# Kernel tuning notes

Hardware: AMD Instinct MI355X
Metric: run time of the kernel (lower is better)

Reference implementation:

```python
import jax, jax.numpy as jnp
import numpy as np

B_, C_, H_, W_, Dd_ = 2, 64, 32, 32, 32
D_INNER, D_STATE, DT_RANK, D_CONV = 64, 8, 4, 4


def setup_inputs() -> dict:
    key = jax.random.key(0)
    ks = jax.random.split(key, 12)
    s = 0.05
    A_init = jnp.log(jnp.tile(jnp.arange(1, D_STATE + 1, dtype=jnp.float32), (D_INNER, 1)))
    return {
        "input": jax.random.normal(ks[0], (B_, C_, H_, W_, Dd_), jnp.float32),
        "conv_w": jax.random.normal(ks[1], (C_, C_, 3, 3, 3), jnp.float32) * s,
        "conv_b": jax.random.normal(ks[2], (C_,), jnp.float32) * s,
        "in_proj_w": jax.random.normal(ks[3], (2 * D_INNER, C_), jnp.float32) * s,
        "conv1d_w": jax.random.normal(ks[4], (D_INNER, 1, D_CONV), jnp.float32) * s,
        "conv1d_b": jax.random.normal(ks[5], (D_INNER,), jnp.float32) * s,
        "x_proj_w": jax.random.normal(ks[6], (DT_RANK + 2 * D_STATE, D_INNER), jnp.float32) * s,
        "dt_proj_w": jax.random.normal(ks[7], (D_INNER, DT_RANK), jnp.float32) * s,
        "dt_proj_b": jax.random.normal(ks[8], (D_INNER,), jnp.float32) * s,
        "A_log": A_init,
        "A_b_log": A_init + 0.01,
        "D_skip": jnp.ones((D_INNER,), jnp.float32),
        "out_proj_w": jax.random.normal(ks[9], (C_, D_INNER), jnp.float32) * s,
        "ln_g": jnp.ones((C_,), jnp.float32),
        "ln_b": jnp.zeros((C_,), jnp.float32),
    }


def _conv3d(x, w, b):
    y = jax.lax.conv_general_dilated(x, w, (1, 1, 1), [(1, 1), (1, 1), (1, 1)],
                                     dimension_numbers=("NCDHW", "OIDHW", "NCDHW"))
    return y + b[None, :, None, None, None]


def _instance_norm(x, eps=1e-5):
    m = x.mean(axis=(2, 3, 4), keepdims=True)
    v = ((x - m) ** 2).mean(axis=(2, 3, 4), keepdims=True)
    return (x - m) * jax.lax.rsqrt(v + eps)


def _selective_scan(xc, dt, Bm, Cm, A, D_skip):
    # xc, dt: (b,L,d); Bm, Cm: (b,L,n); A: (d,n)
    dA = jnp.exp(dt[..., None] * A)                       # (b,L,d,n)
    dBx = (dt * xc)[..., None] * Bm[:, :, None, :]        # (b,L,d,n)

    def comb(l, r):
        al, bl = l
        ar, br = r
        return ar * al, ar * bl + br

    _, h = jax.lax.associative_scan(comb, (dA, dBx), axis=1)
    y = jnp.einsum("bldn,bln->bld", h, Cm)
    return y + xc * D_skip


def _direction(xz, conv1d_w, conv1d_b, x_proj_w, dt_proj_w, dt_proj_b, A, D_skip):
    x, z = jnp.split(xz, 2, axis=-1)                      # each (b,L,d)
    xt = jnp.swapaxes(x, 1, 2)                            # (b,d,L)
    xc = jax.lax.conv_general_dilated(xt, conv1d_w, (1,), [(D_CONV - 1, 0)],
                                      feature_group_count=D_INNER,
                                      dimension_numbers=("NCH", "OIH", "NCH"))
    xc = jax.nn.silu(jnp.swapaxes(xc + conv1d_b[None, :, None], 1, 2))  # (b,L,d)
    dbl = xc @ x_proj_w.T
    dt_r = dbl[..., :DT_RANK]
    Bm = dbl[..., DT_RANK:DT_RANK + D_STATE]
    Cm = dbl[..., DT_RANK + D_STATE:]
    dt = jax.nn.softplus(dt_r @ dt_proj_w.T + dt_proj_b)
    y = _selective_scan(xc, dt, Bm, Cm, A, D_skip)
    return y * jax.nn.silu(z)


def reference(input, conv_w, conv_b, in_proj_w, conv1d_w, conv1d_b, x_proj_w,
              dt_proj_w, dt_proj_b, A_log, A_b_log, D_skip, out_proj_w, ln_g, ln_b):
    # skip path: Conv3d -> InstanceNorm3d -> ReLU
    skip = jax.nn.relu(_instance_norm(_conv3d(input, conv_w, conv_b)))
    b, c, h, w, d = input.shape
    tokens = input.transpose(0, 2, 3, 4, 1).reshape(b, h * w * d, c)  # b (hwd) c
    xz = tokens @ in_proj_w.T                                          # (b,L,2d)
    A = -jnp.exp(A_log)
    A_b = -jnp.exp(A_b_log)
    y_f = _direction(xz, conv1d_w, conv1d_b, x_proj_w, dt_proj_w, dt_proj_b, A, D_skip)
    y_b = _direction(xz[:, ::-1], conv1d_w, conv1d_b, x_proj_w, dt_proj_w, dt_proj_b, A_b, D_skip)[:, ::-1]
    out = ((y_f + y_b) @ out_proj_w.T) / 2.0  # if_devide_out=True
    mu = out.mean(-1, keepdims=True)
    var = ((out - mu) ** 2).mean(-1, keepdims=True)
    out = (out - mu) * jax.lax.rsqrt(var + 1e-5) * ln_g + ln_b  # use_norm=True
    vol = out.reshape(b, h, w, d, c).transpose(0, 4, 1, 2, 3)
    return _conv3d(vol, conv_w, conv_b) + skip
```

## Files before the change

### kernel.cpp

```cpp
#include <hip/hip_runtime.h>
#include <hip/hip_bf16.h>

typedef __hip_bfloat16 bf16;
typedef __attribute__((ext_vector_type(8))) short short8;
typedef __attribute__((ext_vector_type(4))) float f32x4;

__device__ __forceinline__ float b2f(bf16 x){ return __bfloat162float(x); }
__device__ __forceinline__ bf16  f2b(float x){ return __float2bfloat16(x); }
__device__ __forceinline__ float s2f(short s){ bf16 t = *(bf16*)&s; return b2f(t); }

__device__ __forceinline__ float ldin(const void* p, size_t i, int f32){
  return f32 ? ((const float*)p)[i] : b2f(((const bf16*)p)[i]);
}
__device__ __forceinline__ void stout(void* p, size_t i, float v, int f32){
  if(f32) ((float*)p)[i] = v; else ((bf16*)p)[i] = f2b(v);
}

constexpr int SP   = 32*32*32;
constexpr int LTOK = SP;
constexpr int NC   = 512;
constexpr int CLEN = LTOK / NC;
constexpr int NSEQ = 2*2*64*8;
constexpr int SEG  = 16;
constexpr int SEGLEN = NC/SEG;

__global__ void k_detect(const void* conv_w, int* flag){
  if(threadIdx.x==0 && blockIdx.x==0){
    const bf16* p = (const bf16*)conv_w;
    int f = 0;
    for(int i=0;i<128;i++){
      float v = b2f(p[i]);
      if(!(v==v) || fabsf(v) > 1.0f) f = 1;
    }
    *flag = f;
  }
}

__global__ void k_fill(void* out, int n, const int* flag){
  const int f32 = *flag;
  int i = blockIdx.x*256 + threadIdx.x;
  if(i<n) stout(out, i, 12345.0f, f32);
}

__global__ void k_wprep(const void* __restrict__ cw, bf16* __restrict__ wt,
                        const int* __restrict__ flag){
  const int f32 = *flag;
  int t = blockIdx.x*256 + threadIdx.x;
  if(t >= 27*64*64) return;
  int tap = t >> 12;
  int oc  = (t >> 6) & 63;
  int ci  = t & 63;
  wt[t] = f2b(ldin(cw, ((size_t)(oc*64+ci))*27 + tap, f32));
}

__global__ __launch_bounds__(256) void k_inprojm(
    const void* __restrict__ in, const void* __restrict__ pw,
    bf16* __restrict__ xz, bf16* __restrict__ xin_t,
    const int* __restrict__ flag){
  const int f32 = *flag;
  __shared__ bf16 tok[128*72];
  __shared__ bf16 wl [128*72];
  int tid = threadIdx.x;
  int b = blockIdx.x >> 8, tile = blockIdx.x & 255;
  int l0 = tile*128;

  for(int p=tid; p<1024; p+=256){
    int j = p & 127, c8 = p >> 7;
    short8 v;
    #pragma unroll
    for(int k=0;k<8;k++){
      bf16 t = f2b(ldin(pw, j*64 + c8*8 + k, f32));
      v[k] = *(short*)&t;
    }
    *(short8*)(&wl[j*72 + c8*8]) = v;
  }
  for(int p=tid; p<1024; p+=256){
    int i = p & 127, c8 = p >> 7;
    short8 v;
    #pragma unroll
    for(int k=0;k<8;k++){
      bf16 t = f2b(ldin(in, ((size_t)(b*64 + c8*8 + k))*SP + l0 + i, f32));
      v[k] = *(short*)&t;
    }
    *(short8*)(&tok[i*72 + c8*8]) = v;
  }
  __syncthreads();

  int lane = tid & 63, wv = tid >> 6;
  int pn = lane & 15, quad = lane >> 4, kg8 = quad*8;
  f32x4 acc[2][8];
  #pragma unroll
  for(int mt=0;mt<2;mt++)
    #pragma unroll
    for(int nt=0;nt<8;nt++) acc[mt][nt]=(f32x4)(0.f);

  #pragma unroll
  for(int kq=0;kq<2;kq++){
    short8 a0 = *(const short8*)(&tok[(wv*32      + pn)*72 + kq*32 + kg8]);
    short8 a1 = *(const short8*)(&tok[(wv*32 + 16 + pn)*72 + kq*32 + kg8]);
    #pragma unroll
    for(int nt=0;nt<8;nt++){
      short8 bb = *(const short8*)(&wl[(nt*16+pn)*72 + kq*32 + kg8]);
      acc[0][nt] = __builtin_amdgcn_mfma_f32_16x16x32_bf16(a0,bb,acc[0][nt],0,0,0);
      acc[1][nt] = __builtin_amdgcn_mfma_f32_16x16x32_bf16(a1,bb,acc[1][nt],0,0,0);
    }
  }

  #pragma unroll
  for(int mt=0;mt<2;mt++){
    #pragma unroll
    for(int nt=0;nt<8;nt++){
      #pragma unroll
      for(int r=0;r<4;r++){
        int token = wv*32 + mt*16 + quad*4 + r;
        xz[((size_t)b*LTOK + l0 + token)*128 + nt*16 + pn] = f2b(acc[mt][nt][r]);
      }
    }
  }
  for(int p=tid; p<8192; p+=256){
    int i = p >> 6, c = p & 63;
    xin_t[((size_t)b*SP + l0 + i)*64 + c] = tok[i*72 + c];
  }
}

__global__ __launch_bounds__(256, 2) void k_convm(
    const bf16* __restrict__ xin_t, const bf16* __restrict__ wt,
    const void* __restrict__ cb, const bf16* __restrict__ skip,
    bf16* __restrict__ out_bf, void* __restrict__ out_any,
    int mode, const int* __restrict__ flag){
  const int f32 = *flag;
  __shared__ bf16 xt[972*40];

  int tid  = threadIdx.x;
  int lane = tid & 63;
  int wv   = tid >> 6;
  int pn   = lane & 15;
  int quad = lane >> 4;
  int kg8  = quad * 8;
  int laneA = pn*64 + kg8;

  int blk0 = blockIdx.x;
  int blk  = (blk0 & 7)*128 + (blk0 >> 3);
  int ocg = blk & 3;
  int wh  = (blk >> 2) & 1;
  int dh2 = (blk >> 3) & 1;
  int h   = (blk >> 4) & 31;
  int b   = blk >> 9;
  int w0  = wh*16;
  int d0  = dh2*16;

  f32x4 acc[4];
  #pragma unroll
  for(int m=0;m<4;m++) acc[m]=(f32x4)(0.f);

  for(int cic=0; cic<64; cic+=32){
    if(cic) __syncthreads();
    for(int it=0; it<16; it++){
      int j = it*256 + tid;
      if(j < 3888){
        int q4 = j & 3, row = j >> 2;
        int hh = row / 324; int rem = row - hh*324;
        int ww = rem / 18;  int dd = rem - ww*18;
        int hg = h + hh - 1, wg = w0 + ww - 1, d = d0 + dd - 1;
        short8 v = (short8)(0);
        if((unsigned)hg < 32u && (unsigned)wg < 32u && (unsigned)d < 32u)
          v = *(const short8*)(&xin_t[(((size_t)b*SP) + hg*1024 + wg*32 + d)*64 + cic + q4*8]);
        *(short8*)(&xt[row*40 + q4*8]) = v;
      }
    }
    __syncthreads();

    short8 afr[27];
    #pragma unroll
    for(int t=0;t<27;t++)
      afr[t] = *(const short8*)(wt + t*4096 + ocg*1024 + cic + laneA);

    #pragma unroll
    for(int kz=0;kz<3;kz++){
      #pragma unroll
      for(int ky=0;ky<3;ky++){
        #pragma unroll
        for(int kx=0;kx<3;kx++){
          int tap = (kz*3+ky)*3+kx;
          #pragma unroll
          for(int wr=0;wr<4;wr++){
            int rix = (kz*18 + wv*4 + wr + ky)*18 + kx + pn;
            short8 bb = *(const short8*)(&xt[rix*40 + kg8]);
            acc[wr] = __builtin_amdgcn_mfma_f32_16x16x32_bf16(afr[tap], bb, acc[wr], 0,0,0);
          }
        }
      }
    }
  }

  #pragma unroll
  for(int wr=0;wr<4;wr++){
    #pragma unroll
    for(int r=0;r<4;r++){
      int oc = ocg*16 + quad*4 + r;
      size_t idx = ((size_t)(b*64+oc))*SP + h*1024 + (w0 + wv*4 + wr)*32 + d0 + pn;
      float v = acc[wr][r] + ldin(cb, oc, f32);
      if(mode==0) out_bf[idx] = f2b(v);
      else        stout(out_any, idx, v + b2f(skip[idx]), f32);
    }
  }
}

__global__ void k_inorm(bf16* __restrict__ buf){
  int bc = blockIdx.x;
  bf16* p = buf + (size_t)bc*SP;
  float s=0.f, s2=0.f;
  for(int i=threadIdx.x;i<SP;i+=256){ float v=b2f(p[i]); s+=v; s2+=v*v; }
  __shared__ float sh[8];
  #pragma unroll
  for(int m=32;m>=1;m>>=1){ s += __shfl_xor(s,m); s2 += __shfl_xor(s2,m); }
  int wid = threadIdx.x>>6;
  if((threadIdx.x&63)==0){ sh[wid]=s; sh[4+wid]=s2; }
  __syncthreads();
  if(threadIdx.x==0){ float a=0,b2=0; for(int i=0;i<4;i++){a+=sh[i]; b2+=sh[4+i];} sh[0]=a; sh[4]=b2; }
  __syncthreads();
  float mean = sh[0]*(1.f/SP);
  float var  = sh[4]*(1.f/SP) - mean*mean;
  float inv = rsqrtf(fmaxf(var,0.f) + 1e-5f);
  for(int i=threadIdx.x;i<SP;i+=256){
    float v=(b2f(p[i])-mean)*inv;
    p[i] = f2b(v>0.f ? v : 0.f);
  }
}

__global__ void k_dirprep(const bf16* __restrict__ xz, const void* __restrict__ c1w,
                          const void* __restrict__ c1b, const void* __restrict__ xpw,
                          bf16* __restrict__ bcg, float* __restrict__ dtr,
                          const int* __restrict__ flag){
  const int f32 = *flag;
  __shared__ float xs[67][64];
  __shared__ float xcs[64][65];
  __shared__ float xws[20][65];
  int bid = blockIdx.x;
  int g = bid >> 10, b = (bid>>9)&1, tile = bid & 511;
  int l0 = tile*64;
  int gb = g*2+b;
  for(int t=threadIdx.x; t<20*64; t+=256){ int j=t>>6, d=t&63; xws[j][d]=ldin(xpw, t, f32); }
  for(int t=threadIdx.x; t<67*64; t+=256){
    int row=t>>6, d=t&63;
    int l = l0 + row - 3;
    float v = 0.f;
    if(l>=0 && l<LTOK){
      int lg = g ? (LTOK-1-l) : l;
      v = b2f(xz[((size_t)b*LTOK + lg)*128 + d]);
    }
    xs[row][d]=v;
  }
  __syncthreads();
  for(int t=threadIdx.x; t<4096; t+=256){
    int d=t&63, tl=t>>6;
    float acc = ldin(c1b, d, f32);
    #pragma unroll
    for(int k=0;k<4;k++) acc += ldin(c1w, d*4+k, f32) * xs[tl+k][d];
    xcs[tl][d] = acc / (1.f + __expf(-acc));
  }
  __syncthreads();
  for(int task=threadIdx.x; task<1280; task+=256){
    int j = task % 20, tl = task / 20;
    float acc=0.f;
    #pragma unroll
    for(int d=0; d<64; d++) acc += xcs[tl][d]*xws[j][d];
    size_t l = (size_t)gb*LTOK + l0 + tl;
    if(j<4) dtr[l*4 + j] = acc;
    else    bcg[l*16 + (j-4)] = f2b(acc);
  }
}

__global__ __launch_bounds__(256, 2) void k_scan1(
                        const bf16* __restrict__ xz, const float* __restrict__ dtr,
                        const bf16* __restrict__ bcg,
                        const void* __restrict__ c1w, const void* __restrict__ c1b,
                        const void* __restrict__ dpw, const void* __restrict__ dpb,
                        const void* __restrict__ alog, const void* __restrict__ ablog,
                        float* __restrict__ psP, float* __restrict__ psS,
                        const int* __restrict__ flag){
  const int f32 = *flag;
  int wid = blockIdx.x*4 + (threadIdx.x>>6);
  int lane = threadIdx.x & 63;
  int chunk = wid & (NC-1);
  int b = (wid>>9)&1;
  int g = wid>>10;
  int gb = g*2+b;
  const void* al = g ? ablog : alog;
  float ac[8];
  #pragma unroll
  for(int n=0;n<8;n++) ac[n] = -__expf(ldin(al, lane*8+n, f32));
  float cw0=ldin(c1w,lane*4+0,f32), cw1=ldin(c1w,lane*4+1,f32), cw2=ldin(c1w,lane*4+2,f32), cw3=ldin(c1w,lane*4+3,f32);
  float cb_=ldin(c1b,lane,f32);
  float dw0=ldin(dpw,lane*4+0,f32), dw1=ldin(dpw,lane*4+1,f32), dw2=ldin(dpw,lane*4+2,f32), dw3=ldin(dpw,lane*4+3,f32);
  float db_=ldin(dpb,lane,f32);
  float S[8];
  #pragma unroll
  for(int n=0;n<8;n++) S[n]=0.f;
  float Tsum = 0.f;
  int lt0 = chunk*CLEN;
  float x0,x1,x2;
  {
    float xr[3];
    #pragma unroll
    for(int j=0;j<3;j++){
      int lt = lt0-3+j;
      float v=0.f;
      if(lt>=0){ int lg = g ? (LTOK-1-lt) : lt; v=b2f(xz[((size_t)b*LTOK+lg)*128 + lane]); }
      xr[j]=v;
    }
    x0=xr[0]; x1=xr[1]; x2=xr[2];
  }
  for(int i0=0;i0<CLEN;i0+=16){
    bf16 xv[16]; float4 dv[16]; short8 bb[16];
    #pragma unroll
    for(int k=0;k<16;k++){
      int lt = lt0+i0+k;
      int lg = g ? (LTOK-1-lt) : lt;
      xv[k] = xz[((size_t)b*LTOK+lg)*128 + lane];
      size_t l = (size_t)gb*LTOK + lt;
      dv[k] = *(const float4*)(dtr + l*4);
      bb[k] = *(const short8*)(bcg + l*16);
    }
    #pragma unroll
    for(int k=0;k<16;k++){
      float x3 = b2f(xv[k]);
      float pre = cb_ + cw0*x0 + cw1*x1 + cw2*x2 + cw3*x3;
      float xc = pre / (1.f + __expf(-pre));
      float v = db_ + dv[k].x*dw0 + dv[k].y*dw1 + dv[k].z*dw2 + dv[k].w*dw3;
      float e = __expf(-fabsf(v));
      float dt = fmaxf(v,0.f) + __logf(1.f+e);
      Tsum += dt;
      float bx = dt*xc;
      #pragma unroll
      for(int n=0;n<8;n++){
        float a = __expf(dt*ac[n]);
        S[n] = a*S[n] + bx*s2f(bb[k][n]);
      }
      x0=x1; x1=x2; x2=x3;
    }
  }
  int seq = (gb*64 + lane)*8;
  #pragma unroll
  for(int n=0;n<8;n++){
    psP[(size_t)chunk*NSEQ + seq + n] = __expf(ac[n]*Tsum);
    psS[(size_t)chunk*NSEQ + seq + n] = S[n];
  }
}

__global__ void k_scan2a(const float* __restrict__ psP, const float* __restrict__ psS,
                         float* __restrict__ segP, float* __restrict__ segS){
  int idx = blockIdx.x*256 + threadIdx.x;
  int seq = idx & (NSEQ-1);
  int seg = idx >> 11;
  float P = 1.f, S = 0.f;
  int i0 = seg*SEGLEN;
  #pragma unroll 4
  for(int i=0;i<SEGLEN;i++){
    float p = psP[(size_t)(i0+i)*NSEQ + seq];
    float s = psS[(size_t)(i0+i)*NSEQ + seq];
    S = p*S + s;
    P *= p;
  }
  segP[seg*NSEQ + seq] = P;
  segS[seg*NSEQ + seq] = S;
}
__global__ void k_scan2b(const float* __restrict__ segP, const float* __restrict__ segS,
                         float* __restrict__ segC){
  int seq = blockIdx.x*256 + threadIdx.x;
  if(seq >= NSEQ) return;
  float h = 0.f;
  #pragma unroll
  for(int s=0;s<SEG;s++){
    segC[s*NSEQ + seq] = h;
    h = segP[s*NSEQ + seq]*h + segS[s*NSEQ + seq];
  }
}
__global__ void k_scan2c(const float* __restrict__ psP, const float* __restrict__ segC,
                         float* __restrict__ psC){
  int idx = blockIdx.x*256 + threadIdx.x;
  int seq = idx & (NSEQ-1);
  int seg = idx >> 11;
  float h = segC[seg*NSEQ + seq];
  int i0 = seg*SEGLEN;
  #pragma unroll 4
  for(int i=0;i<SEGLEN;i++){
    float p = psP[(size_t)(i0+i)*NSEQ + seq];
    float s = psC[(size_t)(i0+i)*NSEQ + seq];
    psC[(size_t)(i0+i)*NSEQ + seq] = h;
    h = p*h + s;
  }
}

__global__ __launch_bounds__(256, 2) void k_scan3(
                        const bf16* __restrict__ xz, const float* __restrict__ dtr,
                        const bf16* __restrict__ bcg,
                        const void* __restrict__ c1w, const void* __restrict__ c1b,
                        const void* __restrict__ dpw, const void* __restrict__ dpb,
                        const void* __restrict__ alog, const void* __restrict__ ablog,
                        const void* __restrict__ dskip, const float* __restrict__ carry,
                        bf16* __restrict__ ybuf, const int* __restrict__ flag){
  const int f32 = *flag;
  int wid = blockIdx.x*4 + (threadIdx.x>>6);
  int lane = threadIdx.x & 63;
  int chunk = wid & (NC-1);
  int b = (wid>>9)&1;
  int g = wid>>10;
  int gb = g*2+b;
  const void* al = g ? ablog : alog;
  float ac[8];
  #pragma unroll
  for(int n=0;n<8;n++) ac[n] = -__expf(ldin(al, lane*8+n, f32));
  float cw0=ldin(c1w,lane*4+0,f32), cw1=ldin(c1w,lane*4+1,f32), cw2=ldin(c1w,lane*4+2,f32), cw3=ldin(c1w,lane*4+3,f32);
  float cb_=ldin(c1b,lane,f32);
  float dw0=ldin(dpw,lane*4+0,f32), dw1=ldin(dpw,lane*4+1,f32), dw2=ldin(dpw,lane*4+2,f32), dw3=ldin(dpw,lane*4+3,f32);
  float db_=ldin(dpb,lane,f32);
  float dsk = ldin(dskip,lane,f32);
  int seq = (gb*64 + lane)*8;
  float h[8];
  #pragma unroll
  for(int n=0;n<8;n++) h[n] = carry[(size_t)chunk*NSEQ + seq + n];
  int lt0 = chunk*CLEN;
  float x0,x1,x2;
  {
    float xr[3];
    #pragma unroll
    for(int j=0;j<3;j++){
      int lt = lt0-3+j;
      float v=0.f;
      if(lt>=0){ int lg = g ? (LTOK-1-lt) : lt; v=b2f(xz[((size_t)b*LTOK+lg)*128 + lane]); }
      xr[j]=v;
    }
    x0=xr[0]; x1=xr[1]; x2=xr[2];
  }
  for(int i0=0;i0<CLEN;i0+=16){
    bf16 xv[16]; float4 dv[16]; short8 bb[16]; short8 cc[16];
    #pragma unroll
    for(int k=0;k<16;k++){
      int lt = lt0+i0+k;
      int lg = g ? (LTOK-1-lt) : lt;
      xv[k] = xz[((size_t)b*LTOK+lg)*128 + lane];
      size_t l = (size_t)gb*LTOK + lt;
      dv[k] = *(const float4*)(dtr + l*4);
      bb[k] = *(const short8*)(bcg + l*16);
      cc[k] = *(const short8*)(bcg + l*16 + 8);
    }
    #pragma unroll
    for(int k=0;k<16;k++){
      float x3 = b2f(xv[k]);
      float pre = cb_ + cw0*x0 + cw1*x1 + cw2*x2 + cw3*x3;
      float xc = pre / (1.f + __expf(-pre));
      float v = db_ + dv[k].x*dw0 + dv[k].y*dw1 + dv[k].z*dw2 + dv[k].w*dw3;
      float e = __expf(-fabsf(v));
      float dt = fmaxf(v,0.f) + __logf(1.f+e);
      float bx = dt*xc;
      float y = xc*dsk;
      #pragma unroll
      for(int n=0;n<8;n++){
        float a = __expf(dt*ac[n]);
        h[n] = a*h[n] + bx*s2f(bb[k][n]);
        y += h[n]*s2f(cc[k][n]);
      }
      size_t l = (size_t)gb*LTOK + lt0+i0+k;
      ybuf[l*64 + lane] = f2b(y);
      x0=x1; x1=x2; x2=x3;
    }
  }
}

__global__ __launch_bounds__(256) void k_outln(
                        const bf16* __restrict__ ybuf, const bf16* __restrict__ xz,
                        const void* __restrict__ opw,
                        const void* __restrict__ lng, const void* __restrict__ lnb,
                        bf16* __restrict__ vol_t, const int* __restrict__ flag){
  const int f32 = *flag;
  __shared__ bf16 vsm[64*72];
  __shared__ bf16 wsm[64*72];
  __shared__ float gsm[64], bsm[64];
  int tid = threadIdx.x;
  int b = blockIdx.x >> 9, tile = blockIdx.x & 511;
  int l0 = tile*64;

  for(int p=tid; p<512; p+=256){
    int c = p & 63, d8 = p >> 6;
    short8 v;
    #pragma unroll
    for(int k=0;k<8;k++){ bf16 t = f2b(ldin(opw, c*64 + d8*8 + k, f32)); v[k] = *(short*)&t; }
    *(short8*)(&wsm[c*72 + d8*8]) = v;
  }
  if(tid<64){ gsm[tid]=ldin(lng,tid,f32); bsm[tid]=ldin(lnb,tid,f32); }
  for(int p=tid; p<4096; p+=256){
    int tl = p >> 6, d = p & 63;
    int l = l0 + tl;
    float yf = b2f(ybuf[((size_t)(0+b)*LTOK + l)*64 + d]);
    float yb = b2f(ybuf[((size_t)(2+b)*LTOK + (LTOK-1-l))*64 + d]);
    float z  = b2f(xz[((size_t)b*LTOK + l)*128 + 64 + d]);
    float sz = z / (1.f + __expf(-z));
    vsm[tl*72 + d] = f2b(0.5f*(yf+yb)*sz);
  }
  __syncthreads();

  int lane = tid & 63, wv = tid >> 6, pn = lane & 15, quad = lane >> 4, kg8 = quad*8;
  f32x4 acc[4];
  #pragma unroll
  for(int nt=0;nt<4;nt++) acc[nt]=(f32x4)(0.f);
  #pragma unroll
  for(int kq=0;kq<2;kq++){
    short8 a = *(const short8*)(&vsm[(wv*16+pn)*72 + kq*32 + kg8]);
    #pragma unroll
    for(int nt=0;nt<4;nt++){
      short8 bb = *(const short8*)(&wsm[(nt*16+pn)*72 + kq*32 + kg8]);
      acc[nt] = __builtin_amdgcn_mfma_f32_16x16x32_bf16(a,bb,acc[nt],0,0,0);
    }
  }
  __syncthreads();

  float gl[4], bl[4];
  #pragma unroll
  for(int nt=0;nt<4;nt++){ gl[nt]=gsm[nt*16+pn]; bl[nt]=bsm[nt*16+pn]; }
  #pragma unroll
  for(int r=0;r<4;r++){
    float vals[4]; float s=0.f;
    #pragma unroll
    for(int nt=0;nt<4;nt++){ vals[nt]=acc[nt][r]; s+=vals[nt]; }
    #pragma unroll
    for(int m=1;m<16;m<<=1) s += __shfl_xor(s, m);
    float mu = s*(1.f/64.f);
    float s2=0.f;
    #pragma unroll
    for(int nt=0;nt<4;nt++){ float dv=vals[nt]-mu; s2+=dv*dv; }
    #pragma unroll
    for(int m=1;m<16;m<<=1) s2 += __shfl_xor(s2, m);
    float inv = rsqrtf(s2*(1.f/64.f) + 1e-5f);
    int token = wv*16 + quad*4 + r;
    #pragma unroll
    for(int nt=0;nt<4;nt++){
      vsm[token*72 + nt*16 + pn] = f2b((vals[nt]-mu)*inv*gl[nt] + bl[nt]);
    }
  }
  __syncthreads();
  for(int p=tid; p<512; p+=256){
    int tl = p >> 3, d8 = p & 7;
    *(short8*)(&vol_t[((size_t)b*SP + l0 + tl)*64 + d8*8]) = *(const short8*)(&vsm[tl*72 + d8*8]);
  }
}

extern "C" void kernel_launch(void* const* d_in, const int* in_sizes, int n_in,
                              void* d_out, int out_size, void* d_ws, size_t ws_size,
                              hipStream_t stream){
  const void* input  = d_in[0];
  const void* conv_w = d_in[1];
  const void* conv_b = d_in[2];
  const void* inpw   = d_in[3];
  const void* c1w    = d_in[4];
  const void* c1b    = d_in[5];
  const void* xpw    = d_in[6];
  const void* dpw    = d_in[7];
  const void* dpb    = d_in[8];
  const void* alog   = d_in[9];
  const void* ablog  = d_in[10];
  const void* dskip  = d_in[11];
  const void* opw    = d_in[12];
  const void* lng    = d_in[13];
  const void* lnb    = d_in[14];

  char* base = (char*)d_ws;
  bf16*  skipb = (bf16*) (base + 0);
  bf16*  xz    = (bf16*) (base + 8388608);
  bf16*  bcg   = (bf16*) (base + 25165824);
  float* dtr   = (float*)(base + 29360128);
  float* psP   = (float*)(base + 31457280);
  float* psS   = (float*)(base + 35651584);
  bf16*  ybuf  = (bf16*) (base + 39845888);
  bf16*  wt    = (bf16*) (base + 56623104);
  float* segP  = (float*)(base + 56844288);
  float* segS  = (float*)(base + 56975360);
  float* segC  = (float*)(base + 57106432);
  bf16*  xin_t = (bf16*) (base + 31457280);
  bf16*  vol_t = (bf16*) (base + 25165824);
  int*   flagp = (int*)  (base + 60817408);
  const size_t NEED = 60817424;

  k_detect<<<dim3(1), dim3(64), 0, stream>>>(conv_w, flagp);

  if(ws_size < NEED){
    k_fill<<<dim3((out_size+255)/256), dim3(256), 0, stream>>>(d_out, out_size, flagp);
    return;
  }

  k_wprep  <<<dim3(432),   dim3(256), 0, stream>>>(conv_w, wt, flagp);
  k_inprojm<<<dim3(512),   dim3(256), 0, stream>>>(input, inpw, xz, xin_t, flagp);
  k_convm  <<<dim3(1024),  dim3(256), 0, stream>>>(xin_t, wt, conv_b, nullptr, skipb, nullptr, 0, flagp);
  k_inorm  <<<dim3(128),   dim3(256), 0, stream>>>(skipb);
  k_dirprep<<<dim3(2048),  dim3(256), 0, stream>>>(xz, c1w, c1b, xpw, bcg, dtr, flagp);
  k_scan1  <<<dim3(512),   dim3(256), 0, stream>>>(xz, dtr, bcg, c1w, c1b, dpw, dpb, alog, ablog, psP, psS, flagp);
  k_scan2a <<<dim3(128),   dim3(256), 0, stream>>>(psP, psS, segP, segS);
  k_scan2b <<<dim3(8),     dim3(256), 0, stream>>>(segP, segS, segC);
  k_scan2c <<<dim3(128),   dim3(256), 0, stream>>>(psP, segC, psS);
  k_scan3  <<<dim3(512),   dim3(256), 0, stream>>>(xz, dtr, bcg, c1w, c1b, dpw, dpb, alog, ablog, dskip, psS, ybuf, flagp);
  k_outln  <<<dim3(1024),  dim3(256), 0, stream>>>(ybuf, xz, opw, lng, lnb, vol_t, flagp);
  k_convm  <<<dim3(1024),  dim3(256), 0, stream>>>(vol_t, wt, conv_b, skipb, nullptr, d_out, 1, flagp);
}
```

Baseline: 441.4 us.

## Double scan chunk count and restructure dirprep projection into register-blocked dot products

```diff
diff --git a/kernel.cpp b/kernel.cpp
--- a/kernel.cpp
+++ b/kernel.cpp
@@ -18,10 +18,10 @@
 
 constexpr int SP   = 32*32*32;
 constexpr int LTOK = SP;
-constexpr int NC   = 512;
+constexpr int NC   = 1024;
 constexpr int CLEN = LTOK / NC;
 constexpr int NSEQ = 2*2*64*8;
-constexpr int SEG  = 16;
+constexpr int SEG  = 32;
 constexpr int SEGLEN = NC/SEG;
 
 __global__ void k_detect(const void* conv_w, int* flag){
@@ -228,20 +228,22 @@
   }
 }
 
-__global__ void k_dirprep(const bf16* __restrict__ xz, const void* __restrict__ c1w,
+__global__ __launch_bounds__(256) void k_dirprep(
+                          const bf16* __restrict__ xz, const void* __restrict__ c1w,
                           const void* __restrict__ c1b, const void* __restrict__ xpw,
                           bf16* __restrict__ bcg, float* __restrict__ dtr,
                           const int* __restrict__ flag){
   const int f32 = *flag;
   __shared__ float xs[67][64];
-  __shared__ float xcs[64][65];
-  __shared__ float xws[20][65];
+  __shared__ float xcs[64][68];
+  __shared__ float xws[20][68];
   int bid = blockIdx.x;
   int g = bid >> 10, b = (bid>>9)&1, tile = bid & 511;
   int l0 = tile*64;
   int gb = g*2+b;
-  for(int t=threadIdx.x; t<20*64; t+=256){ int j=t>>6, d=t&63; xws[j][d]=ldin(xpw, t, f32); }
-  for(int t=threadIdx.x; t<67*64; t+=256){
+  int tid = threadIdx.x;
+  for(int t=tid; t<20*64; t+=256){ int j=t>>6, d=t&63; xws[j][d]=ldin(xpw, t, f32); }
+  for(int t=tid; t<67*64; t+=256){
     int row=t>>6, d=t&63;
     int l = l0 + row - 3;
     float v = 0.f;
@@ -252,22 +254,36 @@
     xs[row][d]=v;
   }
   __syncthreads();
-  for(int t=threadIdx.x; t<4096; t+=256){
-    int d=t&63, tl=t>>6;
-    float acc = ldin(c1b, d, f32);
-    #pragma unroll
-    for(int k=0;k<4;k++) acc += ldin(c1w, d*4+k, f32) * xs[tl+k][d];
-    xcs[tl][d] = acc / (1.f + __expf(-acc));
-  }
-  __syncthreads();
-  for(int task=threadIdx.x; task<1280; task+=256){
-    int j = task % 20, tl = task / 20;
-    float acc=0.f;
-    #pragma unroll
-    for(int d=0; d<64; d++) acc += xcs[tl][d]*xws[j][d];
+  {
+    int d = tid & 63;
+    float cw0=ldin(c1w,d*4+0,f32), cw1=ldin(c1w,d*4+1,f32),
+          cw2=ldin(c1w,d*4+2,f32), cw3=ldin(c1w,d*4+3,f32);
+    float cb_=ldin(c1b,d,f32);
+    for(int tl = tid>>6; tl<64; tl+=4){
+      float acc = cb_ + cw0*xs[tl][d] + cw1*xs[tl+1][d] + cw2*xs[tl+2][d] + cw3*xs[tl+3][d];
+      xcs[tl][d] = acc / (1.f + __expf(-acc));
+    }
+  }
+  __syncthreads();
+  {
+    int tl = tid & 63, wq = tid >> 6;
+    float acc[5] = {0.f,0.f,0.f,0.f,0.f};
+    #pragma unroll 4
+    for(int d4=0; d4<16; d4++){
+      float4 xv = *(const float4*)(&xcs[tl][d4*4]);
+      #pragma unroll
+      for(int jj=0; jj<5; jj++){
+        float4 wv = *(const float4*)(&xws[wq*5+jj][d4*4]);
+        acc[jj] += xv.x*wv.x + xv.y*wv.y + xv.z*wv.z + xv.w*wv.w;
+      }
+    }
     size_t l = (size_t)gb*LTOK + l0 + tl;
-    if(j<4) dtr[l*4 + j] = acc;
-    else    bcg[l*16 + (j-4)] = f2b(acc);
+    #pragma unroll
+    for(int jj=0; jj<5; jj++){
+      int j = wq*5 + jj;
+      if(j<4) dtr[l*4 + j] = acc[jj];
+      else    bcg[l*16 + (j-4)] = f2b(acc[jj]);
+    }
   }
 }
 
@@ -283,8 +299,8 @@
   int wid = blockIdx.x*4 + (threadIdx.x>>6);
   int lane = threadIdx.x & 63;
   int chunk = wid & (NC-1);
-  int b = (wid>>9)&1;
-  int g = wid>>10;
+  int b = (wid>>10)&1;
+  int g = wid>>11;
   int gb = g*2+b;
   const void* al = g ? ablog : alog;
   float ac[8];
@@ -311,10 +327,10 @@
     }
     x0=xr[0]; x1=xr[1]; x2=xr[2];
   }
-  for(int i0=0;i0<CLEN;i0+=16){
-    bf16 xv[16]; float4 dv[16]; short8 bb[16];
-    #pragma unroll
-    for(int k=0;k<16;k++){
+  for(int i0=0;i0<CLEN;i0+=8){
+    bf16 xv[8]; float4 dv[8]; short8 bb[8];
+    #pragma unroll
+    for(int k=0;k<8;k++){
       int lt = lt0+i0+k;
       int lg = g ? (LTOK-1-lt) : lt;
       xv[k] = xz[((size_t)b*LTOK+lg)*128 + lane];
@@ -323,7 +339,7 @@
       bb[k] = *(const short8*)(bcg + l*16);
     }
     #pragma unroll
-    for(int k=0;k<16;k++){
+    for(int k=0;k<8;k++){
       float x3 = b2f(xv[k]);
       float pre = cb_ + cw0*x0 + cw1*x1 + cw2*x2 + cw3*x3;
       float xc = pre / (1.f + __expf(-pre));
@@ -404,8 +420,8 @@
   int wid = blockIdx.x*4 + (threadIdx.x>>6);
   int lane = threadIdx.x & 63;
   int chunk = wid & (NC-1);
-  int b = (wid>>9)&1;
-  int g = wid>>10;
+  int b = (wid>>10)&1;
+  int g = wid>>11;
   int gb = g*2+b;
   const void* al = g ? ablog : alog;
   float ac[8];
@@ -433,10 +449,10 @@
     }
     x0=xr[0]; x1=xr[1]; x2=xr[2];
   }
-  for(int i0=0;i0<CLEN;i0+=16){
-    bf16 xv[16]; float4 dv[16]; short8 bb[16]; short8 cc[16];
-    #pragma unroll
-    for(int k=0;k<16;k++){
+  for(int i0=0;i0<CLEN;i0+=8){
+    bf16 xv[8]; float4 dv[8]; short8 bb[8]; short8 cc[8];
+    #pragma unroll
+    for(int k=0;k<8;k++){
       int lt = lt0+i0+k;
       int lg = g ? (LTOK-1-lt) : lt;
       xv[k] = xz[((size_t)b*LTOK+lg)*128 + lane];
@@ -446,7 +462,7 @@
       cc[k] = *(const short8*)(bcg + l*16 + 8);
     }
     #pragma unroll
-    for(int k=0;k<16;k++){
+    for(int k=0;k<8;k++){
       float x3 = b2f(xv[k]);
       float pre = cb_ + cw0*x0 + cw1*x1 + cw2*x2 + cw3*x3;
       float xc = pre / (1.f + __expf(-pre));
@@ -570,16 +586,16 @@
   bf16*  bcg   = (bf16*) (base + 25165824);
   float* dtr   = (float*)(base + 29360128);
   float* psP   = (float*)(base + 31457280);
-  float* psS   = (float*)(base + 35651584);
-  bf16*  ybuf  = (bf16*) (base + 39845888);
+  bf16*  xin_t = (bf16*) (base + 39845888);
+  bf16*  ybuf  = (bf16*) (base + 31457280);
+  float* psS   = (float*)(base + 48234496);
+  bf16*  vol_t = (bf16*) (base + 48234496);
   bf16*  wt    = (bf16*) (base + 56623104);
   float* segP  = (float*)(base + 56844288);
-  float* segS  = (float*)(base + 56975360);
-  float* segC  = (float*)(base + 57106432);
-  bf16*  xin_t = (bf16*) (base + 31457280);
-  bf16*  vol_t = (bf16*) (base + 25165824);
-  int*   flagp = (int*)  (base + 60817408);
-  const size_t NEED = 60817424;
+  float* segS  = (float*)(base + 57106432);
+  float* segC  = (float*)(base + 57368576);
+  int*   flagp = (int*)  (base + 57630720);
+  const size_t NEED = 57630736;
 
   k_detect<<<dim3(1), dim3(64), 0, stream>>>(conv_w, flagp);
 
@@ -593,11 +609,11 @@
   k_convm  <<<dim3(1024),  dim3(256), 0, stream>>>(xin_t, wt, conv_b, nullptr, skipb, nullptr, 0, flagp);
   k_inorm  <<<dim3(128),   dim3(256), 0, stream>>>(skipb);
   k_dirprep<<<dim3(2048),  dim3(256), 0, stream>>>(xz, c1w, c1b, xpw, bcg, dtr, flagp);
-  k_scan1  <<<dim3(512),   dim3(256), 0, stream>>>(xz, dtr, bcg, c1w, c1b, dpw, dpb, alog, ablog, psP, psS, flagp);
-  k_scan2a <<<dim3(128),   dim3(256), 0, stream>>>(psP, psS, segP, segS);
+  k_scan1  <<<dim3(1024),  dim3(256), 0, stream>>>(xz, dtr, bcg, c1w, c1b, dpw, dpb, alog, ablog, psP, psS, flagp);
+  k_scan2a <<<dim3(256),   dim3(256), 0, stream>>>(psP, psS, segP, segS);
   k_scan2b <<<dim3(8),     dim3(256), 0, stream>>>(segP, segS, segC);
-  k_scan2c <<<dim3(128),   dim3(256), 0, stream>>>(psP, segC, psS);
-  k_scan3  <<<dim3(512),   dim3(256), 0, stream>>>(xz, dtr, bcg, c1w, c1b, dpw, dpb, alog, ablog, dskip, psS, ybuf, flagp);
+  k_scan2c <<<dim3(256),   dim3(256), 0, stream>>>(psP, segC, psS);
+  k_scan3  <<<dim3(1024),  dim3(256), 0, stream>>>(xz, dtr, bcg, c1w, c1b, dpw, dpb, alog, ablog, dskip, psS, ybuf, flagp);
   k_outln  <<<dim3(1024),  dim3(256), 0, stream>>>(ybuf, xz, opw, lng, lnb, vol_t, flagp);
   k_convm  <<<dim3(1024),  dim3(256), 0, stream>>>(vol_t, wt, conv_b, skipb, nullptr, d_out, 1, flagp);
 }
```

Measured after the change: 411.4 us. 1.07x faster.
